# Kernel optimization log

Measured on AMD Instinct MI355X. Metric: run time of the kernel, lower is better.

The kernel has to match this reference:

```python
import jax, jax.numpy as jnp
from jax import lax
import numpy as np

D = 128          # condition_dim
NUM_STEPS = 1000
FFN = 2048       # torch TransformerEncoderLayer default dim_feedforward


def _conv(x, w, b):
    # 3x3 conv, stride 1, padding 1 (SAME), NCHW / OIHW layout as in torch
    y = lax.conv_general_dilated(x, w, (1, 1), 'SAME',
                                 dimension_numbers=('NCHW', 'OIHW', 'NCHW'))
    return y + b[None, :, None, None]


def _ln(x, g, b):
    m = jnp.mean(x, -1, keepdims=True)
    v = jnp.mean((x - m) ** 2, -1, keepdims=True)
    return (x - m) / jnp.sqrt(v + 1e-5) * g + b


def setup_inputs() -> dict:
    key = jax.random.key(0)
    ks = iter(jax.random.split(key, 40))
    B, C, H, W = 64, 3, 128, 128
    flat = C * H * W
    def rn(shape, scale=0.02):
        return jax.random.normal(next(ks), shape, jnp.float32) * scale
    return dict(
        cond_img=jax.random.normal(next(ks), (B, C, H, W), jnp.float32),
        tgt_img=jax.random.normal(next(ks), (B, C, H, W), jnp.float32),
        noise=jax.random.normal(next(ks), (B, C, H, W), jnp.float32),
        t=jax.random.randint(next(ks), (B,), 0, NUM_STEPS),
        # condition encoder params
        enc_lin_w=rn((D, flat)), enc_lin_b=jnp.zeros((D,), jnp.float32),
        in_w=rn((2, 3 * D, D)), in_b=jnp.zeros((2, 3 * D), jnp.float32),
        out_w=rn((2, D, D)), out_b=jnp.zeros((2, D), jnp.float32),
        ff1_w=rn((2, FFN, D)), ff1_b=jnp.zeros((2, FFN), jnp.float32),
        ff2_w=rn((2, D, FFN)), ff2_b=jnp.zeros((2, D), jnp.float32),
        ln1_g=jnp.ones((2, D), jnp.float32), ln1_b=jnp.zeros((2, D), jnp.float32),
        ln2_g=jnp.ones((2, D), jnp.float32), ln2_b=jnp.zeros((2, D), jnp.float32),
        # SimpleUNet params
        d1_w=rn((32, C, 3, 3)), d1_b=jnp.zeros((32,), jnp.float32),
        d2_w=rn((64, 32, 3, 3)), d2_b=jnp.zeros((64,), jnp.float32),
        mid_w=rn((64, D)), mid_b=jnp.zeros((64,), jnp.float32),
        u1_w=rn((32, 64, 3, 3)), u1_b=jnp.zeros((32,), jnp.float32),
        u2_w=rn((C, 32, 3, 3)), u2_b=jnp.zeros((C,), jnp.float32),
    )


def _forward(cond_img, tgt_img, noise, t,
             enc_lin_w, enc_lin_b, in_w, in_b, out_w, out_b,
             ff1_w, ff1_b, ff2_w, ff2_b, ln1_g, ln1_b, ln2_g, ln2_b,
             d1_w, d1_b, d2_w, d2_b, mid_w, mid_b, u1_w, u1_b, u2_w, u2_b):
    B = cond_img.shape[0]
    # ---- TransformerConditionEncoder (seq_len == 1, eval mode) ----
    x = cond_img.reshape(B, -1) @ enc_lin_w.T + enc_lin_b  # [B, D]
    for i in range(2):
        # self-attention over a length-1 sequence: softmax over one key == 1,
        # so attn(x) == out_proj(v_proj(x)) exactly.
        v = x @ in_w[i][2 * D:3 * D].T + in_b[i][2 * D:3 * D]
        a = v @ out_w[i].T + out_b[i]
        x = _ln(x + a, ln1_g[i], ln1_b[i])
        f = jnp.maximum(x @ ff1_w[i].T + ff1_b[i], 0.0) @ ff2_w[i].T + ff2_b[i]
        x = _ln(x + f, ln2_g[i], ln2_b[i])
    c = x  # [B, D]
    # ---- LinearScheduler.q_sample ----
    betas = jnp.linspace(1e-4, 0.02, NUM_STEPS)
    alpha_bars = jnp.cumprod(1.0 - betas)
    ab = alpha_bars[t][:, None, None, None]
    z_t = jnp.sqrt(ab) * tgt_img + jnp.sqrt(1.0 - ab) * noise
    # ---- SimpleUNet ----
    h = jax.nn.relu(_conv(z_t, d1_w, d1_b))
    h = jax.nn.relu(_conv(h, d2_w, d2_b))
    h = h + (c @ mid_w.T + mid_b)[:, :, None, None]
    h = jax.nn.relu(_conv(h, u1_w, u1_b))
    eps_pred = _conv(h, u2_w, u2_b)
    # ---- MSE loss ----
    return jnp.mean((eps_pred - noise) ** 2)


def reference(cond_img, tgt_img, noise, t,
              enc_lin_w, enc_lin_b, in_w, in_b, out_w, out_b,
              ff1_w, ff1_b, ff2_w, ff2_b, ln1_g, ln1_b, ln2_g, ln2_b,
              d1_w, d1_b, d2_w, d2_b, mid_w, mid_b, u1_w, u1_b, u2_w, u2_b):
    return _forward(cond_img, tgt_img, noise, t,
                    enc_lin_w, enc_lin_b, in_w, in_b, out_w, out_b,
                    ff1_w, ff1_b, ff2_w, ff2_b, ln1_g, ln1_b, ln2_g, ln2_b,
                    d1_w, d1_b, d2_w, d2_b, mid_w, mid_b, u1_w, u1_b, u2_w, u2_b)
```

## Files before the change

### kernel.cpp

```cpp
#include <hip/hip_runtime.h>
#include <math.h>

#define ENC_K 49152
#define KSEG 64
#define KLEN (ENC_K / KSEG)

typedef __attribute__((ext_vector_type(8))) short bf16x8;
typedef __attribute__((ext_vector_type(4))) float f32x4;

__device__ inline unsigned short f2bf(float f) {
    unsigned int u = __builtin_bit_cast(unsigned int, f);
    unsigned int r = u + 0x7fffu + ((u >> 16) & 1u);
    return (unsigned short)(r >> 16);
}
__device__ inline float bf2f(unsigned short h) {
    return __builtin_bit_cast(float, ((unsigned int)h) << 16);
}
__device__ inline float dot4(const float4 a, const float4 b) {
    return a.x * b.x + a.y * b.y + a.z * b.z + a.w * b.w;
}

__global__ void k_alpha(const int* __restrict__ t, float* __restrict__ sab, float* __restrict__ snab) {
    int b = threadIdx.x;
    if (b < 64) {
        int tb = t[b];
        const float step = (0.02f - 1e-4f) / 999.0f;
        float ab = 1.0f;
        for (int i = 0; i <= tb; ++i) {
            float beta = 1e-4f + step * (float)i;
            ab *= (1.0f - beta);
        }
        sab[b] = sqrtf(ab);
        snab[b] = sqrtf(1.0f - ab);
    }
}

__global__ void k_prep_cw(const float* __restrict__ w, unsigned short* __restrict__ out, int CO, int CI) {
    int idx = blockIdx.x * 256 + threadIdx.x;
    int total = CO * CI * 9;
    if (idx < total) {
        int tap = idx / (CO * CI);
        int rem = idx % (CO * CI);
        int co = rem / CI, ci = rem % CI;
        out[idx] = f2bf(w[((size_t)co * CI + ci) * 9 + tap]);
    }
}

__global__ void k_prep_u2(const float* __restrict__ w, unsigned short* __restrict__ out) {
    int idx = blockIdx.x * 256 + threadIdx.x;
    if (idx < 9 * 16 * 32) {
        int tap = idx / 512;
        int rem = idx % 512;
        int co = rem / 32, ci = rem % 32;
        out[idx] = (co < 3) ? f2bf(w[((size_t)co * 32 + ci) * 9 + tap]) : (unsigned short)0;
    }
}

__global__ void k_enc_gemm(const float* __restrict__ cond, const float* __restrict__ w,
                           float* __restrict__ partial) {
    __shared__ float As[16][68];
    __shared__ float Ws[16][68];
    int tid = threadIdx.x;
    int j = tid & 15, i = tid >> 4;
    int d0 = blockIdx.x * 16, b0 = blockIdx.y * 16;
    int k0 = blockIdx.z * KLEN;
    float a0 = 0.f, a1 = 0.f, a2 = 0.f, a3 = 0.f;
    for (int kk = 0; kk < KLEN; kk += 64) {
        for (int idx = tid; idx < 1024; idx += 256) {
            int r = idx >> 6, c = idx & 63;
            As[r][c] = cond[(size_t)(b0 + r) * ENC_K + k0 + kk + c];
            Ws[r][c] = w[(size_t)(d0 + r) * ENC_K + k0 + kk + c];
        }
        __syncthreads();
        const float4* a4 = (const float4*)&As[i][0];
        const float4* w4 = (const float4*)&Ws[j][0];
#pragma unroll
        for (int k = 0; k < 4; ++k) {
            a0 += dot4(a4[k], w4[k]);
            a1 += dot4(a4[k + 4], w4[k + 4]);
            a2 += dot4(a4[k + 8], w4[k + 8]);
            a3 += dot4(a4[k + 12], w4[k + 12]);
        }
        __syncthreads();
    }
    partial[((size_t)blockIdx.z * 64 + b0 + i) * 128 + d0 + j] = (a0 + a1) + (a2 + a3);
}

__global__ void k_enc_reduce(const float* __restrict__ partial, const float* __restrict__ bias,
                             float* __restrict__ x0) {
    int idx = blockIdx.x * 256 + threadIdx.x;
    float s = bias[idx & 127];
    for (int ks = 0; ks < KSEG; ++ks) s += partial[(size_t)ks * 8192 + idx];
    x0[idx] = s;
}

__device__ float sum128(float v, int tid, float* red) {
    if (tid < 128) red[tid] = v;
    __syncthreads();
    if (tid < 64) red[tid] += red[tid + 64]; __syncthreads();
    if (tid < 32) red[tid] += red[tid + 32]; __syncthreads();
    if (tid < 16) red[tid] += red[tid + 16]; __syncthreads();
    if (tid < 8)  red[tid] += red[tid + 8];  __syncthreads();
    if (tid < 4)  red[tid] += red[tid + 4];  __syncthreads();
    if (tid < 2)  red[tid] += red[tid + 2];  __syncthreads();
    if (tid < 1)  red[tid] += red[tid + 1];  __syncthreads();
    float s = red[0];
    __syncthreads();
    return s;
}

__global__ __launch_bounds__(512) void k_tf_attn(
    const float* __restrict__ xs, float* __restrict__ yo,
    const float* __restrict__ in_w, const float* __restrict__ in_b,
    const float* __restrict__ out_w, const float* __restrict__ out_b,
    const float* __restrict__ ln1_g, const float* __restrict__ ln1_b, int L) {
    __shared__ float xr[128], vr[128], tp[4][128], red[128];
    int b = blockIdx.x, tid = threadIdx.x;
    if (tid < 128) xr[tid] = xs[b * 128 + tid];
    __syncthreads();
    int d = tid & 127, s = tid >> 7;
    {
        const float4* w = (const float4*)(in_w + ((size_t)L * 384 + 256 + d) * 128) + s * 8;
        const float4* x4 = (const float4*)xr + s * 8;
        float p = 0.f;
#pragma unroll
        for (int k = 0; k < 8; ++k) p += dot4(x4[k], w[k]);
        tp[s][d] = p;
    }
    __syncthreads();
    if (tid < 128) vr[tid] = in_b[L * 384 + 256 + tid] + tp[0][tid] + tp[1][tid] + tp[2][tid] + tp[3][tid];
    __syncthreads();
    {
        const float4* w = (const float4*)(out_w + ((size_t)L * 128 + d) * 128) + s * 8;
        const float4* v4 = (const float4*)vr + s * 8;
        float p = 0.f;
#pragma unroll
        for (int k = 0; k < 8; ++k) p += dot4(v4[k], w[k]);
        tp[s][d] = p;
    }
    __syncthreads();
    float y = 0.f;
    if (tid < 128) y = xr[tid] + out_b[L * 128 + tid] + tp[0][tid] + tp[1][tid] + tp[2][tid] + tp[3][tid];
    float m1 = sum128(y, tid, red) * (1.f / 128.f);
    float c1 = y - m1;
    float v1 = sum128(c1 * c1, tid, red) * (1.f / 128.f);
    if (tid < 128)
        yo[b * 128 + tid] = c1 * rsqrtf(v1 + 1e-5f) * ln1_g[L * 128 + tid] + ln1_b[L * 128 + tid];
}

__global__ __launch_bounds__(256) void k_tf_ff1(
    const float* __restrict__ yo, float* __restrict__ f1,
    const float* __restrict__ ff1_w, const float* __restrict__ ff1_b, int L) {
    __shared__ float xr[4][128];
    int tid = threadIdx.x;
    int n0 = blockIdx.x * 128, r0 = blockIdx.y * 4;
    for (int e = tid; e < 512; e += 256)
        xr[e >> 7][e & 127] = yo[(r0 + (e >> 7)) * 128 + (e & 127)];
    __syncthreads();
    int j = n0 + (tid & 127);
    int rh = tid >> 7;
    const float4* w = (const float4*)(ff1_w + ((size_t)L * 2048 + j) * 128);
    const float4* xa = (const float4*)xr[rh * 2];
    const float4* xb = (const float4*)xr[rh * 2 + 1];
    float a0 = 0.f, a1 = 0.f;
#pragma unroll 8
    for (int k = 0; k < 32; ++k) {
        float4 wv = w[k];
        a0 += dot4(xa[k], wv);
        a1 += dot4(xb[k], wv);
    }
    float bv = ff1_b[L * 2048 + j];
    f1[(size_t)(r0 + rh * 2) * 2048 + j] = fmaxf(a0 + bv, 0.f);
    f1[(size_t)(r0 + rh * 2 + 1) * 2048 + j] = fmaxf(a1 + bv, 0.f);
}

__global__ __launch_bounds__(128) void k_tf_ff2(
    const float* __restrict__ f1, float* __restrict__ part,
    const float* __restrict__ ff2_w, int L) {
    __shared__ float fr[256];
    int tid = threadIdx.x;
    int ks = blockIdx.x, row = blockIdx.y;
    int k0 = ks * 256;
    for (int e = tid; e < 256; e += 128) fr[e] = f1[(size_t)row * 2048 + k0 + e];
    __syncthreads();
    const float4* w = (const float4*)(ff2_w + ((size_t)L * 128 + tid) * 2048 + k0);
    const float4* f4 = (const float4*)fr;
    float p = 0.f;
#pragma unroll 8
    for (int k = 0; k < 64; ++k) p += dot4(f4[k], w[k]);
    part[((size_t)ks * 64 + row) * 128 + tid] = p;
}

__global__ __launch_bounds__(128) void k_tf_red(
    const float* __restrict__ part, const float* __restrict__ yo,
    float* __restrict__ xs, const float* __restrict__ ff2_b,
    const float* __restrict__ ln2_g, const float* __restrict__ ln2_b, int L) {
    __shared__ float red[128];
    int b = blockIdx.x, tid = threadIdx.x;
    float y2 = yo[b * 128 + tid] + ff2_b[L * 128 + tid];
#pragma unroll
    for (int ks = 0; ks < 8; ++ks) y2 += part[((size_t)ks * 64 + b) * 128 + tid];
    float m2 = sum128(y2, tid, red) * (1.f / 128.f);
    float c2 = y2 - m2;
    float v2 = sum128(c2 * c2, tid, red) * (1.f / 128.f);
    xs[b * 128 + tid] = c2 * rsqrtf(v2 + 1e-5f) * ln2_g[L * 128 + tid] + ln2_b[L * 128 + tid];
}

__global__ void k_mid(const float* __restrict__ xe, const float* __restrict__ mid_w,
                      const float* __restrict__ mid_b, float* __restrict__ mid) {
    int b = blockIdx.x, c = threadIdx.x;
    float s = mid_b[c];
    const float* xr = xe + b * 128;
    const float* wr = mid_w + c * 128;
    for (int k = 0; k < 128; ++k) s += xr[k] * wr[k];
    mid[b * 64 + c] = s;
}

__global__ __launch_bounds__(256, 4) void k_conv1(
    const float* __restrict__ tgt, const float* __restrict__ noise,
    const float* __restrict__ sab, const float* __restrict__ snab,
    const float* __restrict__ wgt, const float* __restrict__ bias,
    unsigned short* __restrict__ h1, int b0) {
    __shared__ float it[3][34][35];
    __shared__ float wt[8][3][9];
    int tid = threadIdx.x;
    int tx = tid & 7, ty = tid >> 3;
    int bx = blockIdx.x, by = blockIdx.y;
    int bl = blockIdx.z >> 2, g = blockIdx.z & 3;
    int bg = b0 + bl, co0 = g * 8;
    float za = sab[bg], zb = snab[bg];
    for (int idx = tid; idx < 3 * 34 * 34; idx += 256) {
        int c = idx / 1156, rem = idx % 1156;
        int yy = rem / 34, xx = rem % 34;
        int gy = by * 32 + yy - 1, gx = bx * 32 + xx - 1;
        float v = 0.f;
        if (gy >= 0 && gy < 128 && gx >= 0 && gx < 128) {
            size_t off = (((size_t)bg * 3 + c) * 128 + gy) * 128 + gx;
            v = za * tgt[off] + zb * noise[off];
        }
        it[c][yy][xx] = v;
    }
    for (int idx = tid; idx < 8 * 27; idx += 256) {
        int co = idx / 27, rem = idx % 27;
        wt[co][rem / 9][rem % 9] = wgt[(size_t)(co0 + co) * 27 + rem];
    }
    __syncthreads();
    float acc[8][4];
#pragma unroll
    for (int co = 0; co < 8; ++co)
#pragma unroll
        for (int p = 0; p < 4; ++p) acc[co][p] = 0.f;
#pragma unroll
    for (int c = 0; c < 3; ++c)
#pragma unroll
        for (int ky = 0; ky < 3; ++ky) {
            float win[6];
#pragma unroll
            for (int i = 0; i < 6; ++i) win[i] = it[c][ty + ky][tx * 4 + i];
#pragma unroll
            for (int kx = 0; kx < 3; ++kx)
#pragma unroll
                for (int co = 0; co < 8; ++co) {
                    float w = wt[co][c][ky * 3 + kx];
#pragma unroll
                    for (int p = 0; p < 4; ++p) acc[co][p] += win[kx + p] * w;
                }
        }
    int gy = by * 32 + ty, gx0 = bx * 32 + tx * 4;
#pragma unroll
    for (int p = 0; p < 4; ++p) {
        ushort4 oa, ob;
#pragma unroll
        for (int co = 0; co < 4; ++co)
            ((unsigned short*)&oa)[co] = f2bf(fmaxf(acc[co][p] + bias[co0 + co], 0.f));
#pragma unroll
        for (int co = 0; co < 4; ++co)
            ((unsigned short*)&ob)[co] = f2bf(fmaxf(acc[co + 4][p] + bias[co0 + co + 4], 0.f));
        size_t o = (((size_t)bl * 128 + gy) * 128 + gx0 + p) * 32 + co0;
        *(ushort4*)(h1 + o) = oa;
        *(ushort4*)(h1 + o + 4) = ob;
    }
}

template <int CIN, int COB, int COUT, int MOUT>
__global__ __launch_bounds__(256, 2) void k_convMg(
    const unsigned short* __restrict__ in, const unsigned short* __restrict__ wb,
    const float* __restrict__ bias, const float* __restrict__ mid,
    unsigned short* __restrict__ out, int b0) {
    const int GROUPS = COUT / (16 * COB);
    __shared__ __align__(16) unsigned short in_t[10 * 34 * 40];
    __shared__ __align__(16) unsigned short w_t[9 * COB * 16 * 40];
    int tid = threadIdx.x;
    int bx = blockIdx.x, by = blockIdx.y;
    int bl = blockIdx.z / GROUPS, g = blockIdx.z % GROUPS;
    int bg = b0 + bl;
    int co0 = g * COB * 16;
    int lane = tid & 63, wv = tid >> 6;
    int l15 = lane & 15, ch = lane >> 4;

    f32x4 acc[2][2][COB];
    f32x4 zf = {0.f, 0.f, 0.f, 0.f};
#pragma unroll
    for (int a = 0; a < 2; ++a)
#pragma unroll
        for (int bq = 0; bq < 2; ++bq)
#pragma unroll
            for (int c = 0; c < COB; ++c) acc[a][bq][c] = zf;

    for (int cs = 0; cs < CIN / 32; ++cs) {
        if (cs) __syncthreads();
        for (int c = tid; c < 10 * 34 * 4; c += 256) {
            int cc = c & 3, pix = c >> 2;
            int xx = pix % 34, yy = pix / 34;
            int gy = by * 8 + yy - 1, gx = bx * 32 + xx - 1;
            bf16x8 v = {0, 0, 0, 0, 0, 0, 0, 0};
            if (gy >= 0 && gy < 128 && gx >= 0 && gx < 128)
                v = *(const bf16x8*)(in + (((size_t)bl * 128 + gy) * 128 + gx) * CIN + cs * 32 + cc * 8);
            *(bf16x8*)(in_t + pix * 40 + cc * 8) = v;
        }
        for (int c = tid; c < 9 * COB * 16 * 4; c += 256) {
            int cc = c & 3, row = c >> 2;
            int tap = row / (COB * 16), co = row % (COB * 16);
            bf16x8 v = *(const bf16x8*)(wb + ((size_t)(tap * COUT + co0 + co)) * CIN + cs * 32 + cc * 8);
            *(bf16x8*)(w_t + row * 40 + cc * 8) = v;
        }
        __syncthreads();
#pragma unroll
        for (int ky = 0; ky < 3; ++ky)
#pragma unroll
            for (int kx = 0; kx < 3; ++kx) {
                int tap = ky * 3 + kx;
                bf16x8 af[COB];
#pragma unroll
                for (int cb = 0; cb < COB; ++cb)
                    af[cb] = *(const bf16x8*)(w_t + (tap * COB * 16 + cb * 16 + l15) * 40 + ch * 8);
#pragma unroll
                for (int yl = 0; yl < 2; ++yl) {
                    int yloc = 2 * wv + yl + ky;
#pragma unroll
                    for (int xt = 0; xt < 2; ++xt) {
                        int xloc = xt * 16 + l15 + kx;
                        bf16x8 bfv = *(const bf16x8*)(in_t + (yloc * 34 + xloc) * 40 + ch * 8);
#pragma unroll
                        for (int cb = 0; cb < COB; ++cb)
                            acc[yl][xt][cb] = __builtin_amdgcn_mfma_f32_16x16x32_bf16(
                                af[cb], bfv, acc[yl][xt][cb], 0, 0, 0);
                    }
                }
            }
    }
#pragma unroll
    for (int yl = 0; yl < 2; ++yl) {
        int gy = by * 8 + 2 * wv + yl;
#pragma unroll
        for (int xt = 0; xt < 2; ++xt) {
            int gx = bx * 32 + xt * 16 + l15;
            size_t pixo = (((size_t)bl * 128 + gy) * 128 + gx) * COUT;
#pragma unroll
            for (int cb = 0; cb < COB; ++cb) {
                int co = co0 + cb * 16 + ch * 4;
                ushort4 o;
#pragma unroll
                for (int r = 0; r < 4; ++r) {
                    float v = acc[yl][xt][cb][r] + bias[co + r];
                    v = fmaxf(v, 0.f);
                    if (MOUT == 2) v += mid[bg * 64 + co + r];
                    ((unsigned short*)&o)[r] = f2bf(v);
                }
                *(ushort4*)(out + pixo + co) = o;
            }
        }
    }
}

__global__ __launch_bounds__(256, 3) void k_u2m(
    const unsigned short* __restrict__ h3, const unsigned short* __restrict__ wbu2,
    const float* __restrict__ u2_b, const float* __restrict__ noise,
    float* __restrict__ partial, int b0) {
    __shared__ __align__(16) unsigned short in_t[340 * 40];
    __shared__ __align__(16) unsigned short w_t[9 * 16 * 40];
    __shared__ float rs[256];
    int tid = threadIdx.x;
    int bx = blockIdx.x, by = blockIdx.y, bl = blockIdx.z;
    int bg = b0 + bl;
    int lane = tid & 63, wv = tid >> 6, l15 = lane & 15, ch = lane >> 4;

    for (int c = tid; c < 340 * 4; c += 256) {
        int cc = c & 3, pix = c >> 2;
        int xx = pix % 34, yy = pix / 34;
        int gy = by * 8 + yy - 1, gx = bx * 32 + xx - 1;
        bf16x8 v = {0, 0, 0, 0, 0, 0, 0, 0};
        if (gy >= 0 && gy < 128 && gx >= 0 && gx < 128)
            v = *(const bf16x8*)(h3 + (((size_t)bl * 128 + gy) * 128 + gx) * 32 + cc * 8);
        *(bf16x8*)(in_t + pix * 40 + cc * 8) = v;
    }
    for (int c = tid; c < 9 * 16 * 4; c += 256) {
        int cc = c & 3, row = c >> 2;
        bf16x8 v = *(const bf16x8*)(wbu2 + (size_t)row * 32 + cc * 8);
        *(bf16x8*)(w_t + row * 40 + cc * 8) = v;
    }
    __syncthreads();

    f32x4 acc[2][2];
    f32x4 zf = {0.f, 0.f, 0.f, 0.f};
    acc[0][0] = zf; acc[0][1] = zf; acc[1][0] = zf; acc[1][1] = zf;
#pragma unroll
    for (int ky = 0; ky < 3; ++ky)
#pragma unroll
        for (int kx = 0; kx < 3; ++kx) {
            int tap = ky * 3 + kx;
            bf16x8 af = *(const bf16x8*)(w_t + (tap * 16 + l15) * 40 + ch * 8);
#pragma unroll
            for (int yl = 0; yl < 2; ++yl) {
                int yloc = 2 * wv + yl + ky;
#pragma unroll
                for (int xt = 0; xt < 2; ++xt) {
                    int xloc = xt * 16 + l15 + kx;
                    bf16x8 bfv = *(const bf16x8*)(in_t + (yloc * 34 + xloc) * 40 + ch * 8);
                    acc[yl][xt] = __builtin_amdgcn_mfma_f32_16x16x32_bf16(af, bfv, acc[yl][xt], 0, 0, 0);
                }
            }
        }
    float ss = 0.f;
    if (ch == 0) {
#pragma unroll
        for (int yl = 0; yl < 2; ++yl) {
            int gy = by * 8 + 2 * wv + yl;
#pragma unroll
            for (int xt = 0; xt < 2; ++xt) {
                int gx = bx * 32 + xt * 16 + l15;
#pragma unroll
                for (int r = 0; r < 3; ++r) {
                    float v = acc[yl][xt][r] + u2_b[r];
                    float d = v - noise[(((size_t)bg * 3 + r) * 128 + gy) * 128 + gx];
                    ss += d * d;
                }
            }
        }
    }
    rs[tid] = ss;
    __syncthreads();
    for (int s = 128; s > 0; s >>= 1) {
        if (tid < s) rs[tid] += rs[tid + s];
        __syncthreads();
    }
    if (tid == 0) partial[bg * 64 + by * 4 + bx] = rs[0];
}

__global__ void k_final(const float* __restrict__ partial, float* __restrict__ out) {
    __shared__ float rs[256];
    int tid = threadIdx.x;
    float s = 0.f;
    for (int i = tid; i < 4096; i += 256) s += partial[i];
    rs[tid] = s;
    __syncthreads();
    for (int st = 128; st > 0; st >>= 1) {
        if (tid < st) rs[tid] += rs[tid + st];
        __syncthreads();
    }
    if (tid == 0) out[0] = rs[0] / 3145728.0f;
}

extern "C" void kernel_launch(void* const* d_in, const int* in_sizes, int n_in,
                              void* d_out, int out_size, void* d_ws, size_t ws_size,
                              hipStream_t stream) {
    const float* cond   = (const float*)d_in[0];
    const float* tgt    = (const float*)d_in[1];
    const float* noise  = (const float*)d_in[2];
    const int*   t      = (const int*)d_in[3];
    const float* enc_w  = (const float*)d_in[4];
    const float* enc_b  = (const float*)d_in[5];
    const float* in_w   = (const float*)d_in[6];
    const float* in_b   = (const float*)d_in[7];
    const float* out_w  = (const float*)d_in[8];
    const float* out_b  = (const float*)d_in[9];
    const float* ff1_w  = (const float*)d_in[10];
    const float* ff1_b  = (const float*)d_in[11];
    const float* ff2_w  = (const float*)d_in[12];
    const float* ff2_b  = (const float*)d_in[13];
    const float* ln1_g  = (const float*)d_in[14];
    const float* ln1_b  = (const float*)d_in[15];
    const float* ln2_g  = (const float*)d_in[16];
    const float* ln2_b  = (const float*)d_in[17];
    const float* d1_w   = (const float*)d_in[18];
    const float* d1_b   = (const float*)d_in[19];
    const float* d2_w   = (const float*)d_in[20];
    const float* d2_b   = (const float*)d_in[21];
    const float* mid_w  = (const float*)d_in[22];
    const float* mid_b  = (const float*)d_in[23];
    const float* u1_w   = (const float*)d_in[24];
    const float* u1_b   = (const float*)d_in[25];
    const float* u2_w   = (const float*)d_in[26];
    const float* u2_b   = (const float*)d_in[27];

    float* ws = (float*)d_ws;
    float* sab     = ws;
    float* snab    = ws + 64;
    float* x0      = ws + 128;
    float* mid     = ws + 16512;
    float* msepart = ws + 86144;
    unsigned short* wb2  = (unsigned short*)(ws + 90240);
    unsigned short* wbu1 = (unsigned short*)(ws + 99456);
    unsigned short* wbu2 = (unsigned short*)(ws + 108672);

    const size_t SMALL = 131072;
    const size_t ENCP = (size_t)KSEG * 8192;
    float* encpart = ws + SMALL;
    float* tfy     = ws + SMALL + ENCP;
    float* tff1    = tfy + 8192;
    float* tfpart  = tff1 + 131072;

    size_t fixed = SMALL + ENCP + 8192 + 131072 + 65536;
    size_t avail = (ws_size / 4 > fixed) ? (ws_size / 4 - fixed) : 0;
    int NB = 1;
    const int cands[7] = {64, 32, 16, 8, 4, 2, 1};
    for (int ci = 0; ci < 7; ++ci) {
        if ((size_t)cands[ci] * 1048576ull <= avail) { NB = cands[ci]; break; }
    }
    unsigned short* hb1 = (unsigned short*)(ws + fixed);
    unsigned short* hb2 = (unsigned short*)(ws + fixed + (size_t)NB * 262144ull);
    unsigned short* hb3 = (unsigned short*)(ws + fixed + (size_t)NB * 786432ull);

    k_alpha<<<1, 64, 0, stream>>>(t, sab, snab);
    k_prep_cw<<<72, 256, 0, stream>>>(d2_w, wb2, 64, 32);
    k_prep_cw<<<72, 256, 0, stream>>>(u1_w, wbu1, 32, 64);
    k_prep_u2<<<18, 256, 0, stream>>>(u2_w, wbu2);
    k_enc_gemm<<<dim3(8, 4, KSEG), 256, 0, stream>>>(cond, enc_w, encpart);
    k_enc_reduce<<<32, 256, 0, stream>>>(encpart, enc_b, x0);
    for (int L = 0; L < 2; ++L) {
        k_tf_attn<<<64, 512, 0, stream>>>(x0, tfy, in_w, in_b, out_w, out_b, ln1_g, ln1_b, L);
        k_tf_ff1<<<dim3(16, 16), 256, 0, stream>>>(tfy, tff1, ff1_w, ff1_b, L);
        k_tf_ff2<<<dim3(8, 64), 128, 0, stream>>>(tff1, tfpart, ff2_w, L);
        k_tf_red<<<64, 128, 0, stream>>>(tfpart, tfy, x0, ff2_b, ln2_g, ln2_b, L);
    }
    k_mid<<<64, 64, 0, stream>>>(x0, mid_w, mid_b, mid);

    for (int cb = 0; cb < 64; cb += NB) {
        k_conv1<<<dim3(4, 4, NB * 4), 256, 0, stream>>>(
            tgt, noise, sab, snab, d1_w, d1_b, hb1, cb);
        k_convMg<32, 4, 64, 2><<<dim3(4, 16, NB), 256, 0, stream>>>(
            hb1, wb2, d2_b, mid, hb2, cb);
        k_convMg<64, 2, 32, 1><<<dim3(4, 16, NB), 256, 0, stream>>>(
            hb2, wbu1, u1_b, nullptr, hb3, cb);
        k_u2m<<<dim3(4, 16, NB), 256, 0, stream>>>(
            hb3, wbu2, u2_b, noise, msepart, cb);
    }

    k_final<<<1, 256, 0, stream>>>(msepart, (float*)d_out);
}
```

Baseline: 428.0 us.

## Move transformer FFN to bf16 MFMA kernels and retile encoder GEMM

Replaces the scalar fp32 FFN1/FFN2 kernels with bf16 MFMA kernels, adding per-call conversion of the FFN weights to bf16 and storing the FFN intermediate in bf16 with a padded row stride. The encoder GEMM is retiled to 32x32 blocks with float4 loads and a 2x2 register tile per thread. The aim is to cut the FFN's FP32 ALU cost and improve data reuse in the encoder GEMM. The trade-offs are reduced precision, extra weight-conversion kernels, and far fewer blocks for the FFN and encoder GEMM.

```diff
diff --git a/kernel.cpp b/kernel.cpp
--- a/kernel.cpp
+++ b/kernel.cpp
@@ -56,34 +56,44 @@
     }
 }
 
+__global__ void k_prep_bf(const float* __restrict__ in, unsigned short* __restrict__ out, int n) {
+    int i = blockIdx.x * 256 + threadIdx.x;
+    if (i < n) out[i] = f2bf(in[i]);
+}
+
 __global__ void k_enc_gemm(const float* __restrict__ cond, const float* __restrict__ w,
                            float* __restrict__ partial) {
-    __shared__ float As[16][68];
-    __shared__ float Ws[16][68];
+    __shared__ float As[32][68];
+    __shared__ float Ws[32][68];
     int tid = threadIdx.x;
     int j = tid & 15, i = tid >> 4;
-    int d0 = blockIdx.x * 16, b0 = blockIdx.y * 16;
+    int d0 = blockIdx.x * 32, b0 = blockIdx.y * 32;
     int k0 = blockIdx.z * KLEN;
-    float a0 = 0.f, a1 = 0.f, a2 = 0.f, a3 = 0.f;
+    float a00 = 0.f, a01 = 0.f, a10 = 0.f, a11 = 0.f;
     for (int kk = 0; kk < KLEN; kk += 64) {
-        for (int idx = tid; idx < 1024; idx += 256) {
-            int r = idx >> 6, c = idx & 63;
-            As[r][c] = cond[(size_t)(b0 + r) * ENC_K + k0 + kk + c];
-            Ws[r][c] = w[(size_t)(d0 + r) * ENC_K + k0 + kk + c];
+        for (int idx = tid; idx < 512; idx += 256) {
+            int r = idx >> 4, c = (idx & 15) << 2;
+            *(float4*)&As[r][c] = *(const float4*)&cond[(size_t)(b0 + r) * ENC_K + k0 + kk + c];
+            *(float4*)&Ws[r][c] = *(const float4*)&w[(size_t)(d0 + r) * ENC_K + k0 + kk + c];
         }
         __syncthreads();
-        const float4* a4 = (const float4*)&As[i][0];
-        const float4* w4 = (const float4*)&Ws[j][0];
-#pragma unroll
-        for (int k = 0; k < 4; ++k) {
-            a0 += dot4(a4[k], w4[k]);
-            a1 += dot4(a4[k + 4], w4[k + 4]);
-            a2 += dot4(a4[k + 8], w4[k + 8]);
-            a3 += dot4(a4[k + 12], w4[k + 12]);
+        const float4* aA = (const float4*)&As[i][0];
+        const float4* aB = (const float4*)&As[i + 16][0];
+        const float4* wA = (const float4*)&Ws[j][0];
+        const float4* wB = (const float4*)&Ws[j + 16][0];
+#pragma unroll
+        for (int k = 0; k < 16; ++k) {
+            float4 av0 = aA[k], av1 = aB[k], wv0 = wA[k], wv1 = wB[k];
+            a00 += dot4(av0, wv0); a01 += dot4(av0, wv1);
+            a10 += dot4(av1, wv0); a11 += dot4(av1, wv1);
         }
         __syncthreads();
     }
-    partial[((size_t)blockIdx.z * 64 + b0 + i) * 128 + d0 + j] = (a0 + a1) + (a2 + a3);
+    size_t base = (size_t)blockIdx.z * 64;
+    partial[(base + b0 + i) * 128 + d0 + j] = a00;
+    partial[(base + b0 + i) * 128 + d0 + j + 16] = a01;
+    partial[(base + b0 + i + 16) * 128 + d0 + j] = a10;
+    partial[(base + b0 + i + 16) * 128 + d0 + j + 16] = a11;
 }
 
 __global__ void k_enc_reduce(const float* __restrict__ partial, const float* __restrict__ bias,
@@ -148,47 +158,66 @@
         yo[b * 128 + tid] = c1 * rsqrtf(v1 + 1e-5f) * ln1_g[L * 128 + tid] + ln1_b[L * 128 + tid];
 }
 
-__global__ __launch_bounds__(256) void k_tf_ff1(
-    const float* __restrict__ yo, float* __restrict__ f1,
-    const float* __restrict__ ff1_w, const float* __restrict__ ff1_b, int L) {
-    __shared__ float xr[4][128];
-    int tid = threadIdx.x;
-    int n0 = blockIdx.x * 128, r0 = blockIdx.y * 4;
-    for (int e = tid; e < 512; e += 256)
-        xr[e >> 7][e & 127] = yo[(r0 + (e >> 7)) * 128 + (e & 127)];
-    __syncthreads();
-    int j = n0 + (tid & 127);
-    int rh = tid >> 7;
-    const float4* w = (const float4*)(ff1_w + ((size_t)L * 2048 + j) * 128);
-    const float4* xa = (const float4*)xr[rh * 2];
-    const float4* xb = (const float4*)xr[rh * 2 + 1];
-    float a0 = 0.f, a1 = 0.f;
-#pragma unroll 8
-    for (int k = 0; k < 32; ++k) {
-        float4 wv = w[k];
-        a0 += dot4(xa[k], wv);
-        a1 += dot4(xb[k], wv);
-    }
-    float bv = ff1_b[L * 2048 + j];
-    f1[(size_t)(r0 + rh * 2) * 2048 + j] = fmaxf(a0 + bv, 0.f);
-    f1[(size_t)(r0 + rh * 2 + 1) * 2048 + j] = fmaxf(a1 + bv, 0.f);
-}
-
-__global__ __launch_bounds__(128) void k_tf_ff2(
-    const float* __restrict__ f1, float* __restrict__ part,
-    const float* __restrict__ ff2_w, int L) {
-    __shared__ float fr[256];
-    int tid = threadIdx.x;
-    int ks = blockIdx.x, row = blockIdx.y;
-    int k0 = ks * 256;
-    for (int e = tid; e < 256; e += 128) fr[e] = f1[(size_t)row * 2048 + k0 + e];
-    __syncthreads();
-    const float4* w = (const float4*)(ff2_w + ((size_t)L * 128 + tid) * 2048 + k0);
-    const float4* f4 = (const float4*)fr;
-    float p = 0.f;
-#pragma unroll 8
-    for (int k = 0; k < 64; ++k) p += dot4(f4[k], w[k]);
-    part[((size_t)ks * 64 + row) * 128 + tid] = p;
+__global__ __launch_bounds__(256, 2) void k_ff1m(
+    const float* __restrict__ yo, const unsigned short* __restrict__ w1b,
+    const float* __restrict__ ff1_b, unsigned short* __restrict__ f1, int L) {
+    __shared__ __align__(16) unsigned short xs[64 * 136];
+    int tid = threadIdx.x;
+    int lane = tid & 63, wv = tid >> 6, l15 = lane & 15, ch = lane >> 4;
+    int n0 = blockIdx.x * 64 + wv * 16;
+    for (int e = tid; e < 8192; e += 256)
+        xs[(e >> 7) * 136 + (e & 127)] = f2bf(yo[e]);
+    __syncthreads();
+    f32x4 acc[4];
+    f32x4 zf = {0.f, 0.f, 0.f, 0.f};
+#pragma unroll
+    for (int rg = 0; rg < 4; ++rg) acc[rg] = zf;
+    const unsigned short* wrow = w1b + ((size_t)L * 2048 + n0 + l15) * 128 + ch * 8;
+#pragma unroll
+    for (int ks = 0; ks < 4; ++ks) {
+        bf16x8 af = *(const bf16x8*)(wrow + ks * 32);
+#pragma unroll
+        for (int rg = 0; rg < 4; ++rg) {
+            bf16x8 bv = *(const bf16x8*)(xs + (rg * 16 + l15) * 136 + ks * 32 + ch * 8);
+            acc[rg] = __builtin_amdgcn_mfma_f32_16x16x32_bf16(af, bv, acc[rg], 0, 0, 0);
+        }
+    }
+#pragma unroll
+    for (int rg = 0; rg < 4; ++rg) {
+        ushort4 o;
+#pragma unroll
+        for (int r = 0; r < 4; ++r)
+            ((unsigned short*)&o)[r] =
+                f2bf(fmaxf(acc[rg][r] + ff1_b[L * 2048 + n0 + ch * 4 + r], 0.f));
+        *(ushort4*)(f1 + (size_t)(rg * 16 + l15) * 2056 + n0 + ch * 4) = o;
+    }
+}
+
+__global__ __launch_bounds__(256, 2) void k_ff2m(
+    const unsigned short* __restrict__ f1, const unsigned short* __restrict__ w2b,
+    float* __restrict__ part, int L) {
+    int tid = threadIdx.x;
+    int lane = tid & 63, wv = tid >> 6, l15 = lane & 15, ch = lane >> 4;
+    int ks = blockIdx.x;
+    int dw = blockIdx.y * 64 + wv * 16;
+    f32x4 acc[4];
+    f32x4 zf = {0.f, 0.f, 0.f, 0.f};
+#pragma unroll
+    for (int rg = 0; rg < 4; ++rg) acc[rg] = zf;
+    const unsigned short* wrow = w2b + ((size_t)L * 128 + dw + l15) * 2048 + ks * 512 + ch * 8;
+    const unsigned short* frow = f1 + ks * 512 + ch * 8;
+#pragma unroll
+    for (int kst = 0; kst < 16; ++kst) {
+        bf16x8 af = *(const bf16x8*)(wrow + kst * 32);
+#pragma unroll
+        for (int rg = 0; rg < 4; ++rg) {
+            bf16x8 bv = *(const bf16x8*)(frow + (size_t)(rg * 16 + l15) * 2056 + kst * 32);
+            acc[rg] = __builtin_amdgcn_mfma_f32_16x16x32_bf16(af, bv, acc[rg], 0, 0, 0);
+        }
+    }
+#pragma unroll
+    for (int rg = 0; rg < 4; ++rg)
+        *(float4*)&part[((size_t)ks * 64 + rg * 16 + l15) * 128 + dw + ch * 4] = *(float4*)&acc[rg];
 }
 
 __global__ __launch_bounds__(128) void k_tf_red(
@@ -199,7 +228,7 @@
     int b = blockIdx.x, tid = threadIdx.x;
     float y2 = yo[b * 128 + tid] + ff2_b[L * 128 + tid];
 #pragma unroll
-    for (int ks = 0; ks < 8; ++ks) y2 += part[((size_t)ks * 64 + b) * 128 + tid];
+    for (int ks = 0; ks < 4; ++ks) y2 += part[((size_t)ks * 64 + b) * 128 + tid];
     float m2 = sum128(y2, tid, red) * (1.f / 128.f);
     float c2 = y2 - m2;
     float v2 = sum128(c2 * c2, tid, red) * (1.f / 128.f);
@@ -506,11 +535,13 @@
     const size_t SMALL = 131072;
     const size_t ENCP = (size_t)KSEG * 8192;
     float* encpart = ws + SMALL;
-    float* tfy     = ws + SMALL + ENCP;
-    float* tff1    = tfy + 8192;
-    float* tfpart  = tff1 + 131072;
-
-    size_t fixed = SMALL + ENCP + 8192 + 131072 + 65536;
+    float* tfy     = encpart + ENCP;
+    unsigned short* tff1 = (unsigned short*)(tfy + 8192);
+    float* tfpart  = tfy + 8192 + 65792;
+    unsigned short* wbf1 = (unsigned short*)(tfpart + 32768);
+    unsigned short* wbf2 = (unsigned short*)(tfpart + 32768 + 262144);
+
+    size_t fixed = SMALL + ENCP + 8192 + 65792 + 32768 + 262144 + 262144;
     size_t avail = (ws_size / 4 > fixed) ? (ws_size / 4 - fixed) : 0;
     int NB = 1;
     const int cands[7] = {64, 32, 16, 8, 4, 2, 1};
@@ -525,12 +556,14 @@
     k_prep_cw<<<72, 256, 0, stream>>>(d2_w, wb2, 64, 32);
     k_prep_cw<<<72, 256, 0, stream>>>(u1_w, wbu1, 32, 64);
     k_prep_u2<<<18, 256, 0, stream>>>(u2_w, wbu2);
-    k_enc_gemm<<<dim3(8, 4, KSEG), 256, 0, stream>>>(cond, enc_w, encpart);
+    k_prep_bf<<<2048, 256, 0, stream>>>(ff1_w, wbf1, 524288);
+    k_prep_bf<<<2048, 256, 0, stream>>>(ff2_w, wbf2, 524288);
+    k_enc_gemm<<<dim3(4, 2, KSEG), 256, 0, stream>>>(cond, enc_w, encpart);
     k_enc_reduce<<<32, 256, 0, stream>>>(encpart, enc_b, x0);
     for (int L = 0; L < 2; ++L) {
         k_tf_attn<<<64, 512, 0, stream>>>(x0, tfy, in_w, in_b, out_w, out_b, ln1_g, ln1_b, L);
-        k_tf_ff1<<<dim3(16, 16), 256, 0, stream>>>(tfy, tff1, ff1_w, ff1_b, L);
-        k_tf_ff2<<<dim3(8, 64), 128, 0, stream>>>(tff1, tfpart, ff2_w, L);
+        k_ff1m<<<32, 256, 0, stream>>>(tfy, wbf1, ff1_b, tff1, L);
+        k_ff2m<<<dim3(4, 2), 256, 0, stream>>>(tff1, wbf2, tfpart, L);
         k_tf_red<<<64, 128, 0, stream>>>(tfpart, tfy, x0, ff2_b, ln2_g, ln2_b, L);
     }
     k_mid<<<64, 64, 0, stream>>>(x0, mid_w, mid_b, mid);
```

Result: faster. 399.2 us (-6.7%).
